# Kernel optimization log

Measured on AMD Instinct MI355X. Metric: run time of the kernel, lower is better.

Reference implementation:

```python
import jax, jax.numpy as jnp
import numpy as np

N = 50000   # nodes
E = 800000  # edges
D = 256     # input_dim == hidden_dim (required by original code path)
O = 32      # output_dim
ALPHA = 0.5      # APPNP teleport
ALPHA_RES = 0.0  # residual mix on output
BETA = 1.0       # neighbor-aggregation scale
EPS = 1e-12


def _l2norm(h):
    # F.normalize(h, p=2, dim=1)
    n = jnp.sqrt(jnp.sum(h * h, axis=1, keepdims=True))
    return h / jnp.maximum(n, EPS)


def _gappnp(x, row, col):
    # GAPPNP with K=1, symmetric normalization, self-loops (APPNP-style step)
    sl = jnp.arange(N, dtype=row.dtype)
    r = jnp.concatenate([row, sl])
    c = jnp.concatenate([col, sl])
    deg = jax.ops.segment_sum(jnp.ones(r.shape, x.dtype), r, num_segments=N)
    dinv = jnp.where(deg > 0, jax.lax.rsqrt(jnp.maximum(deg, 1.0)), 0.0)
    norm = dinv[r] * dinv[c]                      # [E+N]
    agg = jax.ops.segment_sum(norm[:, None] * x[c], r, num_segments=N)  # [N, D]
    h = (1.0 - ALPHA) * BETA * agg + ALPHA * x
    return (1.0 - ALPHA_RES) * h + ALPHA_RES * x


def setup_inputs() -> dict:
    key = jax.random.key(0)
    ks = jax.random.split(key, 8)
    s = 1.0 / np.sqrt(D)
    return {
        "x": jax.random.normal(ks[0], (N, D), dtype=jnp.float32),
        "edge_index": jax.random.randint(ks[1], (2, E), 0, N, dtype=jnp.int32),
        "W0": jax.random.normal(ks[2], (D, D), dtype=jnp.float32) * s,
        "b0": jnp.zeros((D,), jnp.float32),
        "Wn0": jax.random.normal(ks[3], (D, D), dtype=jnp.float32) * s,
        "bn0": jnp.zeros((D,), jnp.float32),
        "W1": jax.random.normal(ks[4], (D, D), dtype=jnp.float32) * s,
        "b1": jnp.zeros((D,), jnp.float32),
        "Wn1": jax.random.normal(ks[5], (D, D), dtype=jnp.float32) * s,
        "bn1": jnp.zeros((D,), jnp.float32),
        "W2": jax.random.normal(ks[6], (D, O), dtype=jnp.float32) * s,
        "b2": jnp.zeros((O,), jnp.float32),
    }


def reference(x, edge_index, W0, b0, Wn0, bn0, W1, b1, Wn1, bn1, W2, b2):
    # eval mode: dropout is identity
    row, col = edge_index[0], edge_index[1]
    h = x
    for (W, b, Wn, bn) in ((W0, b0, Wn0, bn0), (W1, b1, Wn1, bn1)):
        h = h @ W + b                       # fc[c]
        nb = h @ Wn + bn                    # fc_n[c] (separate_neighbors)
        nb = _gappnp(nb, row, col)          # propagate neighbors
        h = h + nb
        h = _l2norm(h)                      # norm == 'normalize'
        h = jax.nn.relu(h)                  # activation 'relu'
    h = h @ W2 + b2                         # final layer, no norm (c != 0)
    return h
```

## Files before the change

### kernel.cpp

```cpp
#include <hip/hip_runtime.h>
#include <hip/hip_bf16.h>

#define NN 50000
#define NE 800000
#define DD 256
#define OO 32
#define EB 3125
#define CASTB 12500
#define BCAP 64

typedef __attribute__((ext_vector_type(8))) short short8;
typedef __attribute__((ext_vector_type(4))) float float4v;

#define AS1 __attribute__((address_space(1)))
#define AS3 __attribute__((address_space(3)))

__device__ __forceinline__ float lo16f(unsigned int u) {
    union { unsigned int i; float f; } x; x.i = u << 16; return x.f;
}
__device__ __forceinline__ float hi16f(unsigned int u) {
    union { unsigned int i; float f; } x; x.i = u & 0xFFFF0000u; return x.f;
}
__device__ __forceinline__ unsigned short f2b(float f) {
    union { float f; unsigned int i; } x;
    x.f = f;
    unsigned int r = x.i + 0x7FFFu + ((x.i >> 16) & 1u);
    return (unsigned short)(r >> 16);
}

__device__ __forceinline__ int pack_idx(int k, int n) {
    return (k >> 5) * 8192 + (n >> 4) * 512 + (((k & 31) >> 3) * 16 + (n & 15)) * 8 + (k & 7);
}

__global__ __launch_bounds__(256) void pre_all(const int* __restrict__ row,
                                               const int* __restrict__ col,
                                               int* __restrict__ cnt,
                                               unsigned short* __restrict__ bucket,
                                               const float* __restrict__ x,
                                               unsigned short* __restrict__ xb,
                                               const float* __restrict__ W0,
                                               const float* __restrict__ Wn0,
                                               const float* __restrict__ W1,
                                               const float* __restrict__ Wn1,
                                               const float* __restrict__ W2,
                                               const float* __restrict__ b0_,
                                               const float* __restrict__ bn0,
                                               const float* __restrict__ b1_,
                                               const float* __restrict__ bn1,
                                               unsigned short* __restrict__ Wp0,
                                               unsigned short* __restrict__ Wp1,
                                               unsigned short* __restrict__ Wt2,
                                               float* __restrict__ bc0,
                                               float* __restrict__ bc1) {
    __shared__ float wrow[256];
    int b = blockIdx.x, t = threadIdx.x;
    if (b < EB) {
        int e = b * 256 + t;
        int r = row[e], c = col[e];
        int p = atomicAdd(&cnt[r], 1);
        if (p < BCAP) bucket[(size_t)r * BCAP + p] = (unsigned short)c;
    } else if (b < EB + 256) {
        int n = b - EB;
        Wp0[pack_idx(t, n)] = f2b(W0[t * 256 + n]);
    } else if (b < EB + 512) {
        int n = b - (EB + 256);
        Wp1[pack_idx(t, n)] = f2b(W1[t * 256 + n]);
    } else if (b < EB + 544) {
        int n = b - (EB + 512);
        Wt2[n * 256 + t] = f2b(W2[t * 32 + n]);
    } else if (b < EB + 800) {
        int k = b - (EB + 544);
        wrow[t] = W0[k * 256 + t];
        __syncthreads();
        float s = 0.f;
#pragma unroll 8
        for (int m = 0; m < 256; ++m) s = fmaf(wrow[m], Wn0[m * 256 + t], s);
        Wp0[pack_idx(k + 256, t)] = f2b(s);
    } else if (b < EB + 1056) {
        int k = b - (EB + 800);
        wrow[t] = W1[k * 256 + t];
        __syncthreads();
        float s = 0.f;
#pragma unroll 8
        for (int m = 0; m < 256; ++m) s = fmaf(wrow[m], Wn1[m * 256 + t], s);
        Wp1[pack_idx(k + 256, t)] = f2b(s);
    } else if (b == EB + 1056) {
        float s0 = bn0[t], s1 = bn1[t];
        for (int m = 0; m < 256; ++m) {
            s0 = fmaf(b0_[m], Wn0[m * 256 + t], s0);
            s1 = fmaf(b1_[m], Wn1[m * 256 + t], s1);
        }
        bc0[t] = s0;
        bc1[t] = s1;
    } else {
        int i = (b - (EB + 1057)) * 256 + t;
        float4 v = ((const float4*)x)[i];
        ushort4 o;
        o.x = f2b(v.x); o.y = f2b(v.y); o.z = f2b(v.z); o.w = f2b(v.w);
        ((ushort4*)xb)[i] = o;
    }
}

__global__ __launch_bounds__(256) void agg_g(const unsigned short* __restrict__ A,
                                             const int* __restrict__ cnt,
                                             const unsigned short* __restrict__ bucket,
                                             unsigned short* __restrict__ G,
                                             float* __restrict__ pv) {
    int wave = threadIdx.x >> 6, lane = threadIdx.x & 63;
    int half = lane >> 5, s = lane & 31;
    int v = blockIdx.x * 4 + wave;
    const uint4* A4 = (const uint4*)A;

    int deg = cnt[v];
    float dv = rsqrtf((float)(deg + 1));
    if (deg > BCAP) deg = BCAP;

    int c = 0;
    float dc = 0.f;
    if (lane < deg) {
        c = bucket[(size_t)v * BCAP + lane];
        dc = rsqrtf((float)(cnt[c] + 1));
    }
    float sdc = dc;

    float a0 = 0.f, a1 = 0.f, a2 = 0.f, a3 = 0.f;
    float a4 = 0.f, a5 = 0.f, a6 = 0.f, a7 = 0.f;

    int pairs4 = (((deg + 1) >> 1) + 3) & ~3;
    for (int j = 0; j < pairs4; j += 4) {
        int ci[4];
        float di[4];
        uint4 u[4];
#pragma unroll
        for (int q = 0; q < 4; ++q) {
            int srcl = 2 * (j + q) + half;
            ci[q] = __shfl(c, srcl);
            di[q] = __shfl(dc, srcl);
        }
#pragma unroll
        for (int q = 0; q < 4; ++q) u[q] = A4[(size_t)ci[q] * 32 + s];
#pragma unroll
        for (int q = 0; q < 4; ++q) {
            a0 = fmaf(di[q], lo16f(u[q].x), a0);
            a1 = fmaf(di[q], hi16f(u[q].x), a1);
            a2 = fmaf(di[q], lo16f(u[q].y), a2);
            a3 = fmaf(di[q], hi16f(u[q].y), a3);
            a4 = fmaf(di[q], lo16f(u[q].z), a4);
            a5 = fmaf(di[q], hi16f(u[q].z), a5);
            a6 = fmaf(di[q], lo16f(u[q].w), a6);
            a7 = fmaf(di[q], hi16f(u[q].w), a7);
        }
    }

    a0 += __shfl_xor(a0, 32); a1 += __shfl_xor(a1, 32);
    a2 += __shfl_xor(a2, 32); a3 += __shfl_xor(a3, 32);
    a4 += __shfl_xor(a4, 32); a5 += __shfl_xor(a5, 32);
    a6 += __shfl_xor(a6, 32); a7 += __shfl_xor(a7, 32);
#pragma unroll
    for (int o = 32; o > 0; o >>= 1) sdc += __shfl_xor(sdc, o);

    if (half == 0) {
        uint4 au = A4[(size_t)v * 32 + s];
        float av[8] = {lo16f(au.x), hi16f(au.x), lo16f(au.y), hi16f(au.y),
                       lo16f(au.z), hi16f(au.z), lo16f(au.w), hi16f(au.w)};
        float aa[8] = {a0, a1, a2, a3, a4, a5, a6, a7};
        unsigned short ov[8];
#pragma unroll
        for (int i = 0; i < 8; ++i)
            ov[i] = f2b(0.5f * dv * (dv * av[i] + aa[i]) + 0.5f * av[i]);
        *(short8*)&G[(size_t)v * 256 + s * 8] = *(short8*)ov;
    }
    if (lane == 0) pv[v] = 0.5f * dv * (dv + sdc) + 0.5f;
}

template <int FINAL>
__global__ __launch_bounds__(256, 2) void gemm512_norm(const unsigned short* __restrict__ A,
                                                       const unsigned short* __restrict__ G,
                                                       const unsigned short* __restrict__ Wp,
                                                       const float* __restrict__ bias,
                                                       const float* __restrict__ biasc,
                                                       const float* __restrict__ pv,
                                                       unsigned short* __restrict__ Out,
                                                       const unsigned short* __restrict__ Wt2,
                                                       const float* __restrict__ b2,
                                                       float* __restrict__ outF,
                                                       int M) {
    __shared__ unsigned short smem[16384];
    __shared__ unsigned short wt2ls[FINAL ? 8192 : 16];
    int tid = threadIdx.x, lane = tid & 63, wave = tid >> 6;
    int fr = lane & 15, quad = lane >> 4, fk = quad * 8;
    int rb = blockIdx.x * 128;

    int r0 = rb + wave * 32 + fr;      if (r0 >= M) r0 = M - 1;
    int r1 = rb + wave * 32 + 16 + fr; if (r1 >= M) r1 = M - 1;
    const unsigned short* ap0 = A + (size_t)r0 * 256 + fk;
    const unsigned short* ap1 = A + (size_t)r1 * 256 + fk;
    const unsigned short* gp0 = G + (size_t)r0 * 256 + fk;
    const unsigned short* gp1 = G + (size_t)r1 * 256 + fk;

    float4v acc[2][16];
#pragma unroll
    for (int i = 0; i < 2; ++i)
#pragma unroll
        for (int j = 0; j < 16; ++j) acc[i][j] = (float4v){0.f, 0.f, 0.f, 0.f};

#pragma unroll
    for (int i = 0; i < 4; ++i) {
        int ch = wave * 4 + i;
        __builtin_amdgcn_global_load_lds((const AS1 void*)(Wp + ch * 512 + lane * 8),
                                         (AS3 void*)&smem[ch * 512], 16, 0, 0);
    }
    short8 a0c = *(const short8*)ap0;
    short8 a1c = *(const short8*)ap1;

    for (int kk = 0; kk < 16; ++kk) {
        __syncthreads();
        int cur = (kk & 1) * 8192;
        if (kk < 15) {
            int nxt = ((kk + 1) & 1) * 8192;
#pragma unroll
            for (int i = 0; i < 4; ++i) {
                int ch = wave * 4 + i;
                __builtin_amdgcn_global_load_lds(
                    (const AS1 void*)(Wp + (kk + 1) * 8192 + ch * 512 + lane * 8),
                    (AS3 void*)&smem[nxt + ch * 512], 16, 0, 0);
            }
        }
        short8 a0n, a1n;
        if (kk < 15) {
            int kn = kk + 1;
            a0n = (kn < 8) ? *(const short8*)(ap0 + kn * 32) : *(const short8*)(gp0 + (kn - 8) * 32);
            a1n = (kn < 8) ? *(const short8*)(ap1 + kn * 32) : *(const short8*)(gp1 + (kn - 8) * 32);
        }
#pragma unroll
        for (int j = 0; j < 16; ++j) {
            short8 b = *(const short8*)&smem[cur + j * 512 + lane * 8];
            acc[0][j] = __builtin_amdgcn_mfma_f32_16x16x32_bf16(a0c, b, acc[0][j], 0, 0, 0);
            acc[1][j] = __builtin_amdgcn_mfma_f32_16x16x32_bf16(a1c, b, acc[1][j], 0, 0, 0);
        }
        a0c = a0n;
        a1c = a1n;
    }

    if (FINAL) {
#pragma unroll
        for (int c = 0; c < 4; ++c) {
            int idx = tid * 4 + c;
            int n = idx >> 5, ch = idx & 31;
            *(short8*)&wt2ls[n * 256 + ((ch ^ (n & 7)) << 3)] =
                *(const short8*)&Wt2[n * 256 + ch * 8];
        }
    }

    float bv[16], bcv[16];
#pragma unroll
    for (int j = 0; j < 16; ++j) {
        bv[j] = bias[j * 16 + fr];
        bcv[j] = biasc[j * 16 + fr];
    }
    float pvr[2][4];
#pragma unroll
    for (int i = 0; i < 2; ++i)
#pragma unroll
        for (int r = 0; r < 4; ++r) {
            int rg = rb + wave * 32 + i * 16 + quad * 4 + r;
            if (rg >= M) rg = M - 1;
            pvr[i][r] = pv[rg];
        }
    float ss[2][4] = {{0.f, 0.f, 0.f, 0.f}, {0.f, 0.f, 0.f, 0.f}};
#pragma unroll
    for (int i = 0; i < 2; ++i)
#pragma unroll
        for (int j = 0; j < 16; ++j)
#pragma unroll
            for (int r = 0; r < 4; ++r) {
                float t = acc[i][j][r] + bv[j] + pvr[i][r] * bcv[j];
                acc[i][j][r] = t;
                ss[i][r] = fmaf(t, t, ss[i][r]);
            }
#pragma unroll
    for (int o = 1; o < 16; o <<= 1)
#pragma unroll
        for (int i = 0; i < 2; ++i)
#pragma unroll
            for (int r = 0; r < 4; ++r) ss[i][r] += __shfl_xor(ss[i][r], o);
    float inv[2][4];
#pragma unroll
    for (int i = 0; i < 2; ++i)
#pragma unroll
        for (int r = 0; r < 4; ++r) inv[i][r] = 1.0f / fmaxf(sqrtf(ss[i][r]), 1e-12f);

#pragma unroll
    for (int rd = 0; rd < 2; ++rd) {
        __syncthreads();
        if ((wave >> 1) == rd) {
#pragma unroll
            for (int i = 0; i < 2; ++i)
#pragma unroll
                for (int j = 0; j < 16; ++j)
#pragma unroll
                    for (int r = 0; r < 4; ++r) {
                        int rw = (wave & 1) * 32 + i * 16 + quad * 4 + r;
                        unsigned short hv = f2b(fmaxf(acc[i][j][r] * inv[i][r], 0.f));
                        if (FINAL) {
                            int e = j * 16 + fr;
                            smem[rw * 256 + (((e >> 3) ^ (rw & 7)) << 3) + (e & 7)] = hv;
                        } else {
                            smem[rw * 256 + j * 16 + fr] = hv;
                        }
                    }
        }
        __syncthreads();
        if (FINAL) {
            float4v a2[2];
            a2[0] = (float4v){0.f, 0.f, 0.f, 0.f};
            a2[1] = (float4v){0.f, 0.f, 0.f, 0.f};
            int hrow = wave * 16 + fr;
#pragma unroll
            for (int kk = 0; kk < 8; ++kk) {
                int chb = kk * 4 + quad;
                short8 af = *(const short8*)&smem[hrow * 256 + ((chb ^ (hrow & 7)) << 3)];
#pragma unroll
                for (int j = 0; j < 2; ++j) {
                    int n = j * 16 + fr;
                    short8 bf = *(const short8*)&wt2ls[n * 256 + ((chb ^ (n & 7)) << 3)];
                    a2[j] = __builtin_amdgcn_mfma_f32_16x16x32_bf16(af, bf, a2[j], 0, 0, 0);
                }
            }
#pragma unroll
            for (int j = 0; j < 2; ++j) {
                int colg = j * 16 + fr;
                float bb = b2[colg];
#pragma unroll
                for (int r = 0; r < 4; ++r) {
                    int gr = rb + rd * 64 + wave * 16 + quad * 4 + r;
                    if (gr < M) outF[(size_t)gr * 32 + colg] = a2[j][r] + bb;
                }
            }
        } else {
#pragma unroll
            for (int b = 0; b < 8; ++b) {
                int chunk = b * 256 + tid;
                int rw = chunk >> 5, part = chunk & 31;
                int gr = rb + rd * 64 + rw;
                if (gr < M)
                    *(short8*)&Out[(size_t)gr * 256 + part * 8] =
                        *(const short8*)&smem[rw * 256 + part * 8];
            }
        }
    }
}

extern "C" void kernel_launch(void* const* d_in, const int* in_sizes, int n_in,
                              void* d_out, int out_size, void* d_ws, size_t ws_size,
                              hipStream_t stream) {
    const float* x   = (const float*)d_in[0];
    const int* edge  = (const int*)d_in[1];
    const float* W0  = (const float*)d_in[2];
    const float* b0  = (const float*)d_in[3];
    const float* Wn0 = (const float*)d_in[4];
    const float* bn0 = (const float*)d_in[5];
    const float* W1  = (const float*)d_in[6];
    const float* b1  = (const float*)d_in[7];
    const float* Wn1 = (const float*)d_in[8];
    const float* bn1 = (const float*)d_in[9];
    const float* W2  = (const float*)d_in[10];
    const float* b2  = (const float*)d_in[11];
    float* out = (float*)d_out;

    const int N = NN, E = NE;
    const int* row = edge;
    const int* col = edge + E;

    char* p = (char*)d_ws;
    unsigned short* Xbf = (unsigned short*)p; p += (size_t)N * DD * 2;
    unsigned short* Gbf = (unsigned short*)p; p += (size_t)N * DD * 2;
    unsigned short* Abf = (unsigned short*)p; p += (size_t)N * DD * 2;
    unsigned short* Wp0 = (unsigned short*)p; p += 16 * 8192 * 2;
    unsigned short* Wp1 = (unsigned short*)p; p += 16 * 8192 * 2;
    unsigned short* Wt2 = (unsigned short*)p; p += 32 * 256 * 2;
    float* bc0   = (float*)p; p += 256 * 4;
    float* bc1   = (float*)p; p += 256 * 4;
    float* pv    = (float*)p; p += (size_t)N * 4;
    int* cnt     = (int*)p; p += (size_t)N * 4;
    unsigned short* bucket = (unsigned short*)p; p += (size_t)N * BCAP * 2;

    hipMemsetAsync(cnt, 0, (size_t)N * sizeof(int), stream);

    pre_all<<<EB + 1057 + CASTB, 256, 0, stream>>>(row, col, cnt, bucket, x, Xbf,
                                                   W0, Wn0, W1, Wn1, W2,
                                                   b0, bn0, b1, bn1,
                                                   Wp0, Wp1, Wt2, bc0, bc1);

    const int gTiles = (N + 127) / 128;
    agg_g<<<N / 4, 256, 0, stream>>>(Xbf, cnt, bucket, Gbf, pv);
    gemm512_norm<0><<<gTiles, 256, 0, stream>>>(Xbf, Gbf, Wp0, b0, bc0, pv, Abf,
                                                Wt2, b2, out, N);
    agg_g<<<N / 4, 256, 0, stream>>>(Abf, cnt, bucket, Gbf, pv);
    gemm512_norm<1><<<gTiles, 256, 0, stream>>>(Abf, Gbf, Wp1, b1, bc1, pv, Xbf,
                                                Wt2, b2, out, N);
}
```

Before: 326.7 us.

## Double LDS weight stage to two K-chunks per barrier and single-pass epilogue

Result: slower. 335.6 us (+2.7%).

```diff
diff --git a/kernel.cpp b/kernel.cpp
--- a/kernel.cpp
+++ b/kernel.cpp
@@ -185,7 +185,7 @@
                                                        const float* __restrict__ b2,
                                                        float* __restrict__ outF,
                                                        int M) {
-    __shared__ unsigned short smem[16384];
+    __shared__ unsigned short smem[32768];
     __shared__ unsigned short wt2ls[FINAL ? 8192 : 16];
     int tid = threadIdx.x, lane = tid & 63, wave = tid >> 6;
     int fr = lane & 15, quad = lane >> 4, fk = quad * 8;
@@ -205,38 +205,46 @@
         for (int j = 0; j < 16; ++j) acc[i][j] = (float4v){0.f, 0.f, 0.f, 0.f};
 
 #pragma unroll
-    for (int i = 0; i < 4; ++i) {
-        int ch = wave * 4 + i;
+    for (int i = 0; i < 8; ++i) {
+        int ch = wave * 8 + i;
         __builtin_amdgcn_global_load_lds((const AS1 void*)(Wp + ch * 512 + lane * 8),
                                          (AS3 void*)&smem[ch * 512], 16, 0, 0);
     }
     short8 a0c = *(const short8*)ap0;
     short8 a1c = *(const short8*)ap1;
 
-    for (int kk = 0; kk < 16; ++kk) {
+    for (int kk2 = 0; kk2 < 8; ++kk2) {
         __syncthreads();
-        int cur = (kk & 1) * 8192;
-        if (kk < 15) {
-            int nxt = ((kk + 1) & 1) * 8192;
-#pragma unroll
-            for (int i = 0; i < 4; ++i) {
-                int ch = wave * 4 + i;
+        int cur = (kk2 & 1) * 16384;
+        if (kk2 < 7) {
+            int nxt = ((kk2 + 1) & 1) * 16384;
+#pragma unroll
+            for (int i = 0; i < 8; ++i) {
+                int ch = wave * 8 + i;
                 __builtin_amdgcn_global_load_lds(
-                    (const AS1 void*)(Wp + (kk + 1) * 8192 + ch * 512 + lane * 8),
+                    (const AS1 void*)(Wp + (kk2 + 1) * 16384 + ch * 512 + lane * 8),
                     (AS3 void*)&smem[nxt + ch * 512], 16, 0, 0);
             }
         }
+        int k1i = 2 * kk2 + 1, k2i = 2 * kk2 + 2;
+        short8 a0m = *(const short8*)((k1i < 8) ? (ap0 + k1i * 32) : (gp0 + (k1i - 8) * 32));
+        short8 a1m = *(const short8*)((k1i < 8) ? (ap1 + k1i * 32) : (gp1 + (k1i - 8) * 32));
         short8 a0n, a1n;
-        if (kk < 15) {
-            int kn = kk + 1;
-            a0n = (kn < 8) ? *(const short8*)(ap0 + kn * 32) : *(const short8*)(gp0 + (kn - 8) * 32);
-            a1n = (kn < 8) ? *(const short8*)(ap1 + kn * 32) : *(const short8*)(gp1 + (kn - 8) * 32);
+        if (kk2 < 7) {
+            a0n = *(const short8*)((k2i < 8) ? (ap0 + k2i * 32) : (gp0 + (k2i - 8) * 32));
+            a1n = *(const short8*)((k2i < 8) ? (ap1 + k2i * 32) : (gp1 + (k2i - 8) * 32));
         }
 #pragma unroll
         for (int j = 0; j < 16; ++j) {
             short8 b = *(const short8*)&smem[cur + j * 512 + lane * 8];
             acc[0][j] = __builtin_amdgcn_mfma_f32_16x16x32_bf16(a0c, b, acc[0][j], 0, 0, 0);
             acc[1][j] = __builtin_amdgcn_mfma_f32_16x16x32_bf16(a1c, b, acc[1][j], 0, 0, 0);
+        }
+#pragma unroll
+        for (int j = 0; j < 16; ++j) {
+            short8 b = *(const short8*)&smem[cur + 8192 + j * 512 + lane * 8];
+            acc[0][j] = __builtin_amdgcn_mfma_f32_16x16x32_bf16(a0m, b, acc[0][j], 0, 0, 0);
+            acc[1][j] = __builtin_amdgcn_mfma_f32_16x16x32_bf16(a1m, b, acc[1][j], 0, 0, 0);
         }
         a0c = a0n;
         a1c = a1n;
@@ -290,32 +298,31 @@
 #pragma unroll
         for (int r = 0; r < 4; ++r) inv[i][r] = 1.0f / fmaxf(sqrtf(ss[i][r]), 1e-12f);
 
-#pragma unroll
-    for (int rd = 0; rd < 2; ++rd) {
-        __syncthreads();
-        if ((wave >> 1) == rd) {
-#pragma unroll
-            for (int i = 0; i < 2; ++i)
-#pragma unroll
-                for (int j = 0; j < 16; ++j)
-#pragma unroll
-                    for (int r = 0; r < 4; ++r) {
-                        int rw = (wave & 1) * 32 + i * 16 + quad * 4 + r;
-                        unsigned short hv = f2b(fmaxf(acc[i][j][r] * inv[i][r], 0.f));
-                        if (FINAL) {
-                            int e = j * 16 + fr;
-                            smem[rw * 256 + (((e >> 3) ^ (rw & 7)) << 3) + (e & 7)] = hv;
-                        } else {
-                            smem[rw * 256 + j * 16 + fr] = hv;
-                        }
-                    }
-        }
-        __syncthreads();
-        if (FINAL) {
+    __syncthreads();
+#pragma unroll
+    for (int i = 0; i < 2; ++i)
+#pragma unroll
+        for (int j = 0; j < 16; ++j)
+#pragma unroll
+            for (int r = 0; r < 4; ++r) {
+                int rw = wave * 32 + i * 16 + quad * 4 + r;
+                unsigned short hv = f2b(fmaxf(acc[i][j][r] * inv[i][r], 0.f));
+                if (FINAL) {
+                    int e = j * 16 + fr;
+                    smem[rw * 256 + (((e >> 3) ^ (rw & 7)) << 3) + (e & 7)] = hv;
+                } else {
+                    smem[rw * 256 + j * 16 + fr] = hv;
+                }
+            }
+    __syncthreads();
+
+    if (FINAL) {
+#pragma unroll
+        for (int i = 0; i < 2; ++i) {
             float4v a2[2];
             a2[0] = (float4v){0.f, 0.f, 0.f, 0.f};
             a2[1] = (float4v){0.f, 0.f, 0.f, 0.f};
-            int hrow = wave * 16 + fr;
+            int hrow = wave * 32 + i * 16 + fr;
 #pragma unroll
             for (int kk = 0; kk < 8; ++kk) {
                 int chb = kk * 4 + quad;
@@ -333,20 +340,20 @@
                 float bb = b2[colg];
 #pragma unroll
                 for (int r = 0; r < 4; ++r) {
-                    int gr = rb + rd * 64 + wave * 16 + quad * 4 + r;
+                    int gr = rb + wave * 32 + i * 16 + quad * 4 + r;
                     if (gr < M) outF[(size_t)gr * 32 + colg] = a2[j][r] + bb;
                 }
             }
-        } else {
-#pragma unroll
-            for (int b = 0; b < 8; ++b) {
-                int chunk = b * 256 + tid;
-                int rw = chunk >> 5, part = chunk & 31;
-                int gr = rb + rd * 64 + rw;
-                if (gr < M)
-                    *(short8*)&Out[(size_t)gr * 256 + part * 8] =
-                        *(const short8*)&smem[rw * 256 + part * 8];
-            }
+        }
+    } else {
+#pragma unroll
+        for (int b = 0; b < 16; ++b) {
+            int chunk = b * 256 + tid;
+            int rw = chunk >> 5, part = chunk & 31;
+            int gr = rb + rw;
+            if (gr < M)
+                *(short8*)&Out[(size_t)gr * 256 + part * 8] =
+                    *(const short8*)&smem[rw * 256 + part * 8];
         }
     }
 }
```
